# Optimization experiments

Measured on AMD Instinct MI355X. Metric: run time of the kernel, lower is better.

Reference implementation:

```python
import jax, jax.numpy as jnp
import numpy as np

BATCH = 8192
VOCAB = 16384
EMBED = 256
EPS = 1e-6


def setup_inputs() -> dict:
    key = jax.random.key(0)
    k1, k2 = jax.random.split(key)
    # multi-hot indicator input: values in {0,1}; only nonzero positions matter
    x = jax.random.randint(k1, (BATCH, VOCAB), 0, 2, dtype=jnp.int32)
    # learned embedding table (nn.Embedding weight)
    emb = jax.random.normal(k2, (VOCAB, EMBED), dtype=jnp.float32)
    return {"x": x, "emb": emb}


def reference(x, emb):
    # torch: gather embeddings at nonzero (row, col) pairs, scatter-add per row,
    # divide by per-row nonzero count (+eps). Equivalent jit-friendly form:
    # mask @ emb gives the per-row sum of embeddings over nonzero columns.
    mask = (x != 0).astype(emb.dtype)               # [B, V]
    embed_sum = mask @ emb                           # [B, E]
    count = jnp.sum(mask, axis=1, keepdims=True) + EPS  # [B, 1]
    return embed_sum / count
```

## Files before the change

### kernel.cpp

```cpp
#include <hip/hip_runtime.h>
#include <hip/hip_bf16.h>
#include <stdint.h>

#define BATCH 8192
#define VOCAB 16384
#define EMBED 256

#define BM 64
#define BK 64
#define KSPLIT 8
#define KRANGE (VOCAB / KSPLIT)
#define KITERS (KRANGE / BK)
#define MTILES (BATCH / BM)

typedef __attribute__((ext_vector_type(4))) float    f32x4;
typedef __attribute__((ext_vector_type(4))) int      i32x4;
typedef __attribute__((ext_vector_type(4))) unsigned u32x4;

#define EMB_WS_BYTES ((size_t)VOCAB * EMBED * 2)
#define CNT_WS_BYTES ((size_t)KSPLIT * BATCH * 4)
#define PART_STRIDE  ((size_t)BATCH * EMBED)

__device__ __forceinline__ void gload_lds16(const void* g, void* l) {
    __builtin_amdgcn_global_load_lds(
        (const __attribute__((address_space(1))) unsigned int*)(uintptr_t)g,
        (__attribute__((address_space(3))) unsigned int*)(uint32_t)(uintptr_t)l,
        16, 0, 0);
}

__device__ __forceinline__ void mfma_bf16(f32x4& acc, i32x4 a, i32x4 b) {
    asm("v_mfma_f32_16x16x32_bf16 %0, %1, %2, %0" : "+v"(acc) : "v"(a), "v"(b));
}

__global__ __launch_bounds__(256) void prep_kernel(
    const float* __restrict__ emb, unsigned short* __restrict__ emb_ws)
{
    int t = blockIdx.x * 256 + threadIdx.x;
    int ko = t >> 8;
    int e  = t & 255;
    union { unsigned short s[8]; u32x4 q; } v;
    #pragma unroll
    for (int j = 0; j < 8; ++j) {
        float f = emb[(size_t)(ko * 8 + j) * EMBED + e];
        unsigned u = __float_as_uint(f);
        u += 0x7FFFu + ((u >> 16) & 1u);
        v.s[j] = (unsigned short)(u >> 16);
    }
    int kt  = ko >> 3;
    int kk0 = (ko & 7) * 8;
    unsigned byt = (unsigned)(e * 128 + ((kk0 * 2) ^ ((e & 7) << 4)));
    *(u32x4*)((char*)emb_ws + (size_t)kt * 32768 + byt) = v.q;
}

__device__ __forceinline__ void stage_B(const char* bbase, int kt, char* bs, int tid) {
    const char* src = bbase + (size_t)kt * 32768 + tid * 16;
    #pragma unroll
    for (int i = 0; i < 8; ++i)
        gload_lds16(src + i * 4096, bs + tid * 16 + i * 4096);
}

__device__ __forceinline__ void load_A(const int* aptr, int kt, i32x4 (&av)[4]) {
    const int* ap = aptr + kt * BK;
    #pragma unroll
    for (int j = 0; j < 4; ++j) av[j] = *(const i32x4*)(ap + j * 16);
}

__device__ __forceinline__ void pack_A(const i32x4 (&av)[4], char* as_buf,
                                       int ar, int aq, int& cnt, bool docnt) {
    #pragma unroll
    for (int j = 0; j < 4; ++j) {
        unsigned lo = (av[j].x ? 0x3F80u : 0u) | (av[j].y ? 0x3F800000u : 0u);
        unsigned hi = (av[j].z ? 0x3F80u : 0u) | (av[j].w ? 0x3F800000u : 0u);
        if (docnt)
            cnt += (av[j].x != 0) + (av[j].y != 0) + (av[j].z != 0) + (av[j].w != 0);
        int kk = aq * 4 + j * 16;
        unsigned byt = (unsigned)(ar * 128 + ((kk * 2) ^ ((ar & 7) << 4)));
        *(uint2*)(as_buf + byt) = make_uint2(lo, hi);
    }
}

__device__ __forceinline__ void compute_tile(const char* as_buf, const char* bs_buf,
                                             int lane, int wave, f32x4 (&acc)[4][4]) {
    #pragma unroll
    for (int ks = 0; ks < 2; ++ks) {
        int kg = ks * 32 + (lane >> 4) * 8;
        i32x4 af[4], bf[4];
        #pragma unroll
        for (int fm = 0; fm < 4; ++fm) {
            int row = fm * 16 + (lane & 15);
            af[fm] = *(const i32x4*)(as_buf + row * 128 + ((kg * 2) ^ ((row & 7) << 4)));
        }
        #pragma unroll
        for (int fe = 0; fe < 4; ++fe) {
            int e = wave * 64 + fe * 16 + (lane & 15);
            bf[fe] = *(const i32x4*)(bs_buf + e * 128 + ((kg * 2) ^ ((e & 7) << 4)));
        }
        #pragma unroll
        for (int fm = 0; fm < 4; ++fm)
            #pragma unroll
            for (int fe = 0; fe < 4; ++fe)
                mfma_bf16(acc[fm][fe], af[fm], bf[fe]);
    }
}

#define PIPE_BARRIER() do {                                   \
    __builtin_amdgcn_sched_barrier(0);                        \
    asm volatile("s_waitcnt vmcnt(4) lgkmcnt(0)" ::: "memory"); \
    __builtin_amdgcn_sched_barrier(0);                        \
    __builtin_amdgcn_s_barrier();                             \
    __builtin_amdgcn_sched_barrier(0);                        \
} while (0)

__global__ __launch_bounds__(256, 2) void gemm_kernel(
    const int* __restrict__ x, const unsigned short* __restrict__ emb_ws,
    float* __restrict__ part_ws, int* __restrict__ cnt_ws)
{
    __shared__ __align__(16) unsigned short As[2][BM * BK];
    __shared__ __align__(16) unsigned short Bs[2][EMBED * BK];

    int bid   = blockIdx.x;
    int split = bid & (KSPLIT - 1);
    int mt    = bid >> 3;
    int rot   = (bid * 5) & (KITERS - 1);

    int tid  = threadIdx.x;
    int lane = tid & 63;
    int wave = tid >> 6;

    int ar = tid >> 2;
    int aq = tid & 3;
    const int*  aptr  = x + (size_t)(mt * BM + ar) * VOCAB + split * KRANGE + aq * 4;
    const char* bbase = (const char*)emb_ws + (size_t)split * KITERS * 32768;

    int cnt = 0;
    f32x4 acc[4][4];
    #pragma unroll
    for (int i = 0; i < 4; ++i)
        #pragma unroll
        for (int j = 0; j < 4; ++j) acc[i][j] = (f32x4){0.f, 0.f, 0.f, 0.f};

    i32x4 av[4];

    load_A(aptr, rot, av);
    stage_B(bbase, rot, (char*)Bs[0], tid);
    pack_A(av, (char*)As[0], ar, aq, cnt, true);
    __builtin_amdgcn_sched_barrier(0);
    load_A(aptr, (rot + 1) & (KITERS - 1), av);
    PIPE_BARRIER();

    int cur = 0;
    for (int t = 0; t < KITERS; ++t) {
        int tB = (rot + t + 1) & (KITERS - 1);
        stage_B(bbase, tB, (char*)Bs[cur ^ 1], tid);
        __builtin_amdgcn_sched_barrier(0);
        compute_tile((const char*)As[cur], (const char*)Bs[cur], lane, wave, acc);
        pack_A(av, (char*)As[cur ^ 1], ar, aq, cnt, t + 1 < KITERS);
        __builtin_amdgcn_sched_barrier(0);
        int tA = (rot + t + 2) & (KITERS - 1);
        load_A(aptr, tA, av);
        PIPE_BARRIER();
        cur ^= 1;
    }

    cnt += __shfl_xor(cnt, 1);
    cnt += __shfl_xor(cnt, 2);
    if (aq == 0) cnt_ws[split * BATCH + mt * BM + ar] = cnt;

    #pragma unroll
    for (int fm = 0; fm < 4; ++fm)
        #pragma unroll
        for (int fe = 0; fe < 4; ++fe)
            asm volatile("s_nop 7\n\ts_nop 7" : "+v"(acc[fm][fe]));

    float* part = part_ws + (size_t)split * PART_STRIDE;
    #pragma unroll
    for (int fm = 0; fm < 4; ++fm) {
        int row = mt * BM + fm * 16 + (lane >> 4) * 4;
        #pragma unroll
        for (int fe = 0; fe < 4; ++fe) {
            int col = wave * 64 + fe * 16 + (lane & 15);
            float* p = part + (size_t)row * EMBED + col;
            #pragma unroll
            for (int r = 0; r < 4; ++r)
                p[(size_t)r * EMBED] = acc[fm][fe][r];
        }
    }
}

__global__ __launch_bounds__(256) void div_kernel(
    float* __restrict__ out, const float* __restrict__ part_ws,
    const int* __restrict__ cnt_ws)
{
    int t = blockIdx.x * 256 + threadIdx.x;
    int b = t >> 6;
    int c = 0;
    #pragma unroll
    for (int s = 0; s < KSPLIT; ++s) c += cnt_ws[s * BATCH + b];
    float inv = 1.0f / ((float)c + 1e-6f);
    f32x4 v = (f32x4){0.f, 0.f, 0.f, 0.f};
    #pragma unroll
    for (int s = 0; s < KSPLIT; ++s) {
        f32x4 p = ((const f32x4*)(part_ws + s * PART_STRIDE))[t];
        v.x += p.x; v.y += p.y; v.z += p.z; v.w += p.w;
    }
    v.x *= inv; v.y *= inv; v.z *= inv; v.w *= inv;
    ((f32x4*)out)[t] = v;
}

extern "C" void kernel_launch(void* const* d_in, const int* in_sizes, int n_in,
                              void* d_out, int out_size, void* d_ws, size_t ws_size,
                              hipStream_t stream)
{
    const int*   x   = (const int*)d_in[0];
    const float* emb = (const float*)d_in[1];
    float*       out = (float*)d_out;

    unsigned short* emb_ws  = (unsigned short*)d_ws;
    int*            cnt_ws  = (int*)((char*)d_ws + EMB_WS_BYTES);
    float*          part_ws = (float*)((char*)d_ws + EMB_WS_BYTES + CNT_WS_BYTES);

    prep_kernel<<<2048, 256, 0, stream>>>(emb, emb_ws);
    gemm_kernel<<<MTILES * KSPLIT, 256, 0, stream>>>(x, emb_ws, part_ws, cnt_ws);
    div_kernel<<<2048, 256, 0, stream>>>(out, part_ws, cnt_ws);
}
```

Baseline: 765.9 us.

## Single-buffer LDS tiles to fit four GEMM blocks per CU

Replaces the double-buffered A/B LDS ping-pong with single buffers and adds a second barrier per iteration. This halves LDS per block so launch bounds can request four resident blocks per CU instead of two. The goal is to hide global-load latency through occupancy rather than software prefetch. In exchange, each block now stalls on its own loads before computing and pays an extra barrier. The tighter register budget per thread could also cause spills.

```diff
diff --git a/kernel.cpp b/kernel.cpp
--- a/kernel.cpp
+++ b/kernel.cpp
@@ -66,13 +66,12 @@
 }
 
 __device__ __forceinline__ void pack_A(const i32x4 (&av)[4], char* as_buf,
-                                       int ar, int aq, int& cnt, bool docnt) {
+                                       int ar, int aq, int& cnt) {
     #pragma unroll
     for (int j = 0; j < 4; ++j) {
         unsigned lo = (av[j].x ? 0x3F80u : 0u) | (av[j].y ? 0x3F800000u : 0u);
         unsigned hi = (av[j].z ? 0x3F80u : 0u) | (av[j].w ? 0x3F800000u : 0u);
-        if (docnt)
-            cnt += (av[j].x != 0) + (av[j].y != 0) + (av[j].z != 0) + (av[j].w != 0);
+        cnt += (av[j].x != 0) + (av[j].y != 0) + (av[j].z != 0) + (av[j].w != 0);
         int kk = aq * 4 + j * 16;
         unsigned byt = (unsigned)(ar * 128 + ((kk * 2) ^ ((ar & 7) << 4)));
         *(uint2*)(as_buf + byt) = make_uint2(lo, hi);
@@ -103,20 +102,22 @@
     }
 }
 
+#define SBAR() __builtin_amdgcn_sched_barrier(0)
+
 #define PIPE_BARRIER() do {                                   \
-    __builtin_amdgcn_sched_barrier(0);                        \
+    SBAR();                                                   \
     asm volatile("s_waitcnt vmcnt(4) lgkmcnt(0)" ::: "memory"); \
-    __builtin_amdgcn_sched_barrier(0);                        \
+    SBAR();                                                   \
     __builtin_amdgcn_s_barrier();                             \
-    __builtin_amdgcn_sched_barrier(0);                        \
+    SBAR();                                                   \
 } while (0)
 
-__global__ __launch_bounds__(256, 2) void gemm_kernel(
+__global__ __launch_bounds__(256, 4) void gemm_kernel(
     const int* __restrict__ x, const unsigned short* __restrict__ emb_ws,
     float* __restrict__ part_ws, int* __restrict__ cnt_ws)
 {
-    __shared__ __align__(16) unsigned short As[2][BM * BK];
-    __shared__ __align__(16) unsigned short Bs[2][EMBED * BK];
+    __shared__ __align__(16) unsigned short As[BM * BK];
+    __shared__ __align__(16) unsigned short Bs[EMBED * BK];
 
     int bid   = blockIdx.x;
     int split = bid & (KSPLIT - 1);
@@ -140,26 +141,22 @@
         for (int j = 0; j < 4; ++j) acc[i][j] = (f32x4){0.f, 0.f, 0.f, 0.f};
 
     i32x4 av[4];
-
     load_A(aptr, rot, av);
-    stage_B(bbase, rot, (char*)Bs[0], tid);
-    pack_A(av, (char*)As[0], ar, aq, cnt, true);
-    __builtin_amdgcn_sched_barrier(0);
-    load_A(aptr, (rot + 1) & (KITERS - 1), av);
-    PIPE_BARRIER();
-
-    int cur = 0;
+    SBAR();
+
     for (int t = 0; t < KITERS; ++t) {
-        int tB = (rot + t + 1) & (KITERS - 1);
-        stage_B(bbase, tB, (char*)Bs[cur ^ 1], tid);
-        __builtin_amdgcn_sched_barrier(0);
-        compute_tile((const char*)As[cur], (const char*)Bs[cur], lane, wave, acc);
-        pack_A(av, (char*)As[cur ^ 1], ar, aq, cnt, t + 1 < KITERS);
-        __builtin_amdgcn_sched_barrier(0);
-        int tA = (rot + t + 2) & (KITERS - 1);
-        load_A(aptr, tA, av);
+        int tile = (rot + t) & (KITERS - 1);
+        stage_B(bbase, tile, (char*)Bs, tid);
+        SBAR();
+        pack_A(av, (char*)As, ar, aq, cnt);
+        SBAR();
+        int tn = (rot + t + 1) & (KITERS - 1);
+        load_A(aptr, tn, av);
         PIPE_BARRIER();
-        cur ^= 1;
+        compute_tile((const char*)As, (const char*)Bs, lane, wave, acc);
+        SBAR();
+        __builtin_amdgcn_s_barrier();
+        SBAR();
     }
 
     cnt += __shfl_xor(cnt, 1);
```

New measurement: 771.4 us. Within noise of the previous version (+0.7%).
